# Optimization experiments

Hardware: AMD Instinct MI355X
Metric: run time of the kernel (lower is better)

## Reference

```python
import jax, jax.numpy as jnp
import numpy as np

B, T, L, D = 2, 16, 256, 1152
NH, HD = 16, 72
MLP_H = int(int(D * 4.0) * 2 / 3)  # 3072, per SwiGLUFFN


def _rms(x, w, eps=1e-6):
    return x * jax.lax.rsqrt(jnp.mean(jnp.square(x), axis=-1, keepdims=True) + eps) * w


def _attn(x, qkv_w, qkv_b, qn, kn, proj_w, proj_b, nh):
    Bn, N, C = x.shape
    hd = C // nh
    qkv = (x @ qkv_w + qkv_b).reshape(Bn, N, 3, nh, hd)
    qkv = jnp.transpose(qkv, (2, 0, 3, 1, 4))  # [3, Bn, nh, N, hd]
    q, k, v = qkv[0], qkv[1], qkv[2]
    q = _rms(q, qn)
    k = _rms(k, kn)
    scores = jnp.einsum('bhnd,bhmd->bhnm', q, k) / jnp.sqrt(jnp.float32(hd))
    a = jax.nn.softmax(scores, axis=-1)
    o = jnp.einsum('bhnm,bhmd->bhnd', a, v)
    o = jnp.transpose(o, (0, 2, 1, 3)).reshape(Bn, N, C)
    return o @ proj_w + proj_b


def setup_inputs() -> dict:
    key = jax.random.key(0)
    ks = jax.random.split(key, 12)
    w = lambda k, shape: jax.random.normal(k, shape, jnp.float32) * 0.02
    return {
        'x': jax.random.normal(ks[0], (B, T, L, D), jnp.float32),
        'c': jax.random.normal(ks[1], (B, D), jnp.float32),
        'norm1_w': jnp.ones((D,), jnp.float32),
        'norm2_w': jnp.ones((D,), jnp.float32),
        'norm3_w': jnp.ones((D,), jnp.float32),
        'qn_s': jnp.ones((HD,), jnp.float32),
        'kn_s': jnp.ones((HD,), jnp.float32),
        'qkv_s_w': w(ks[2], (D, 3 * D)),
        'qkv_s_b': jnp.zeros((3 * D,), jnp.float32),
        'proj_s_w': w(ks[3], (D, D)),
        'proj_s_b': jnp.zeros((D,), jnp.float32),
        'qn_t': jnp.ones((HD,), jnp.float32),
        'kn_t': jnp.ones((HD,), jnp.float32),
        'qkv_t_w': w(ks[4], (D, 3 * D)),
        'qkv_t_b': jnp.zeros((3 * D,), jnp.float32),
        'proj_t_w': w(ks[5], (D, D)),
        'proj_t_b': jnp.zeros((D,), jnp.float32),
        'w12_w': w(ks[6], (D, 2 * MLP_H)),
        'w12_b': jnp.zeros((2 * MLP_H,), jnp.float32),
        'w3_w': w(ks[7], (MLP_H, D)),
        'w3_b': jnp.zeros((D,), jnp.float32),
        'ada_w': w(ks[8], (D, 9 * D)),
        'ada_b': jnp.zeros((9 * D,), jnp.float32),
    }


def reference(x, c, norm1_w, norm2_w, norm3_w,
              qn_s, kn_s, qkv_s_w, qkv_s_b, proj_s_w, proj_s_b,
              qn_t, kn_t, qkv_t_w, qkv_t_b, proj_t_w, proj_t_b,
              w12_w, w12_b, w3_w, w3_b, ada_w, ada_b):
    Bb, Tt, Ll, Dd = x.shape
    # adaLN_modulation: SiLU then Linear, chunk into 9 [B, D] tensors
    ch = (jax.nn.silu(c) @ ada_w + ada_b).reshape(Bb, 9, Dd)
    sh_s, sc_s, g_s = ch[:, 0], ch[:, 1], ch[:, 2]
    sh_t, sc_t, g_t = ch[:, 3], ch[:, 4], ch[:, 5]
    sh_m, sc_m, g_m = ch[:, 6], ch[:, 7], ch[:, 8]

    # spatial attention over L, folded batch B*T
    x_s = x.reshape(Bb * Tt, Ll, Dd)
    shs = jnp.repeat(sh_s, Tt, axis=0)[:, None, :]   # [B*T,1,D]
    scs = jnp.repeat(sc_s, Tt, axis=0)[:, None, :]
    gs = jnp.repeat(g_s, Tt, axis=0)[:, None, :]
    xn = _rms(x_s, norm1_w) * (1 + scs) + shs
    x_s = x_s + gs * _attn(xn, qkv_s_w, qkv_s_b, qn_s, kn_s, proj_s_w, proj_s_b, NH)
    x = x_s.reshape(Bb, Tt, Ll, Dd)

    # temporal attention over T, folded batch B*L
    x_t = jnp.transpose(x, (0, 2, 1, 3)).reshape(Bb * Ll, Tt, Dd)
    sht = jnp.repeat(sh_t, Ll, axis=0)[:, None, :]
    sct = jnp.repeat(sc_t, Ll, axis=0)[:, None, :]
    gt = jnp.repeat(g_t, Ll, axis=0)[:, None, :]
    xn = _rms(x_t, norm2_w) * (1 + sct) + sht
    x_t = x_t + gt * _attn(xn, qkv_t_w, qkv_t_b, qn_t, kn_t, proj_t_w, proj_t_b, NH)
    x = jnp.transpose(x_t.reshape(Bb, Ll, Tt, Dd), (0, 2, 1, 3))

    # SwiGLU MLP with adaLN modulate + gate
    xn = _rms(x, norm3_w) * (1 + sc_m[:, None, None, :]) + sh_m[:, None, None, :]
    x12 = xn @ w12_w + w12_b
    x1, x2 = jnp.split(x12, 2, axis=-1)
    mlp_out = (jax.nn.silu(x1) * x2) @ w3_w + w3_b
    x = x + g_m[:, None, None, :] * mlp_out
    return x
```

## Files before the change

### kernel.cpp

```cpp
#include <hip/hip_runtime.h>
#include <stdint.h>

typedef __bf16 bf16x8 __attribute__((ext_vector_type(8)));
typedef float f32x4 __attribute__((ext_vector_type(4)));

__device__ __forceinline__ float b2f(uint32_t u) {
  union { uint32_t i; float f; } v; v.i = u << 16; return v.f;
}
__device__ __forceinline__ uint16_t f2b(float f) {
  union { float f; uint32_t i; } v; v.f = f;
  uint32_t r = (v.i + 0x7fffu + ((v.i >> 16) & 1u)) >> 16;
  return (uint16_t)r;
}
__device__ __forceinline__ void unpack8(uint4 u, float* f) {
  f[0] = b2f(u.x & 0xffffu); f[1] = b2f(u.x >> 16);
  f[2] = b2f(u.y & 0xffffu); f[3] = b2f(u.y >> 16);
  f[4] = b2f(u.z & 0xffffu); f[5] = b2f(u.z >> 16);
  f[6] = b2f(u.w & 0xffffu); f[7] = b2f(u.w >> 16);
}

__device__ __forceinline__ void gl2lds16(const void* g, void* l) {
  __builtin_amdgcn_global_load_lds(
      (const __attribute__((address_space(1))) void*)g,
      (__attribute__((address_space(3))) void*)l, 16, 0, 0);
}

__global__ __launch_bounds__(256) void gemm_k(
    const uint16_t* __restrict__ A, int lda,
    const uint16_t* __restrict__ Bt,
    const float* __restrict__ bias,
    uint16_t* __restrict__ outb,
    float* __restrict__ outf, const float* __restrict__ resid,
    const float* __restrict__ gate,
    int N, int K, int mode)
{
  __shared__ __align__(16) uint16_t As[2][128 * 32];
  __shared__ __align__(16) uint16_t Bs[2][128 * 32];
  const int tid = threadIdx.x;
  const int xcd = blockIdx.x & 7;
  const int slot = blockIdx.x >> 3;
  const int mt = xcd * 8 + (slot & 7);
  const int nt = slot >> 3;
  const int row0 = mt * 128, col0 = nt * 128;

  const int lane = tid & 63, wave = tid >> 6;
  const int l15 = lane & 15, quad = lane >> 4;
  const int wm = (wave & 1) * 64, wn = (wave >> 1) * 64;

  f32x4 acc[4][4];
  const f32x4 zero = {0.f, 0.f, 0.f, 0.f};
  for (int i = 0; i < 4; i++)
    for (int j = 0; j < 4; j++)
      acc[i][j] = zero;

  const int rseg = wave * 32 + (lane >> 2);
  const int kseg8 = (((lane & 3) ^ ((lane >> 2) & 3) ^ ((lane >> 4) & 3))) * 8;
  const uint16_t* gA = A + (size_t)(row0 + rseg) * lda + kseg8;
  const uint16_t* gB = Bt + (size_t)(col0 + rseg) * K + kseg8;
  const size_t rowA16 = (size_t)16 * lda;
  const size_t rowB16 = (size_t)16 * K;
  const int woff = wave * 2048;

  const int gsw = ((quad ^ (l15 & 3) ^ ((l15 >> 2) & 3))) * 8;

  gl2lds16(gA,          (char*)As[0] + woff);
  gl2lds16(gA + rowA16, (char*)As[0] + woff + 1024);
  gl2lds16(gB,          (char*)Bs[0] + woff);
  gl2lds16(gB + rowB16, (char*)Bs[0] + woff + 1024);

  for (int k0 = 0; k0 < K; k0 += 32) {
    const int cur = (k0 >> 5) & 1;
    __syncthreads();
    if (k0 + 32 < K) {
      const int nxt = cur ^ 1;
      gl2lds16(gA + k0 + 32,          (char*)As[nxt] + woff);
      gl2lds16(gA + rowA16 + k0 + 32, (char*)As[nxt] + woff + 1024);
      gl2lds16(gB + k0 + 32,          (char*)Bs[nxt] + woff);
      gl2lds16(gB + rowB16 + k0 + 32, (char*)Bs[nxt] + woff + 1024);
    }

    bf16x8 af[4], bfr[4];
#pragma unroll
    for (int i = 0; i < 4; i++) {
      af[i]  = *(const bf16x8*)&As[cur][(wm + i * 16 + l15) * 32 + gsw];
      bfr[i] = *(const bf16x8*)&Bs[cur][(wn + i * 16 + l15) * 32 + gsw];
    }
#pragma unroll
    for (int mi = 0; mi < 4; mi++)
#pragma unroll
      for (int ni = 0; ni < 4; ni++)
        acc[mi][ni] = __builtin_amdgcn_mfma_f32_16x16x32_bf16(af[mi], bfr[ni], acc[mi][ni], 0, 0, 0);
  }

#pragma unroll
  for (int mi = 0; mi < 4; mi++) {
#pragma unroll
    for (int ni = 0; ni < 4; ni++) {
      const int colg = col0 + wn + ni * 16 + l15;
      const float bv = bias ? bias[colg] : 0.f;
#pragma unroll
      for (int i = 0; i < 4; i++) {
        const int rowg = row0 + wm + mi * 16 + quad * 4 + i;
        const float v = acc[mi][ni][i] + bv;
        const size_t idx = (size_t)rowg * N + colg;
        if (mode == 0) {
          outb[idx] = f2b(v);
        } else {
          const int b = rowg >> 12;
          outf[idx] = resid[idx] + gate[b * 10368 + colg] * v;
        }
      }
    }
  }
}

__global__ __launch_bounds__(512, 2) void gemm256_k(
    const uint16_t* __restrict__ A, int lda,
    const uint16_t* __restrict__ Bt,
    const float* __restrict__ bias,
    uint16_t* __restrict__ outb,
    int N, int K)
{
  __shared__ __align__(16) uint16_t L[65536];
  const int tid = threadIdx.x;
  const int lane = tid & 63, wave = tid >> 6;
  const int l15 = lane & 15, quad = lane >> 4;
  const int wm = (wave >> 2) * 128, wn = (wave & 3) * 64;

  const int xcd = blockIdx.x & 7;
  const int slot = blockIdx.x >> 3;
  const int mt = xcd * 4 + (slot & 3);
  const int nt = slot >> 2;
  const int row0 = mt * 256, col0 = nt * 256;

  const int NTk = K >> 6;

  const uint16_t* Ag = A + (size_t)row0 * lda;
  const uint16_t* Bg = Bt + (size_t)col0 * K;

  const int sX = (lane & 7) ^ (lane >> 3);
  const int laneRowA = lane >> 3;
  const int laneK8A = sX * 8;
  const int laneRowB = 2 * (lane >> 3) + ((sX >> 2) & 1);
  const int laneK8B = (sX & 3) * 8;
  const int rA0 = ((wave * 16) & 63) + (((wave * 16) >> 6) << 7);
  const int rB0 = wave * 32;

#define STAGE_A(BUF, SUB, KT) do { \
    const uint16_t* g_ = Ag + (size_t)(rA0 + (SUB) * 64 + laneRowA) * lda + (size_t)(KT) * 64 + laneK8A; \
    uint16_t* l_ = (uint16_t*)&L[(BUF) * 32768 + (rA0 + (SUB) * 64) * 64]; \
    gl2lds16(g_, l_); \
    gl2lds16(g_ + (size_t)8 * lda, l_ + 512); \
  } while (0)

#define STAGE_B(BUF, HALF, KT) do { \
    const uint16_t* g_ = Bg + (size_t)(rB0 + laneRowB) * K + (size_t)(KT) * 64 + (HALF) * 32 + laneK8B; \
    uint16_t* l_ = (uint16_t*)&L[(BUF) * 32768 + 16384 + (HALF) * 8192 + rB0 * 32]; \
    gl2lds16(g_, l_); \
    gl2lds16(g_ + (size_t)16 * K, l_ + 512); \
  } while (0)

  f32x4 acc[8][4];
#pragma unroll
  for (int i = 0; i < 8; i++)
#pragma unroll
    for (int j = 0; j < 4; j++)
      acc[i][j] = (f32x4){0.f, 0.f, 0.f, 0.f};

  bf16x8 a_[4], b_[4];

#define PHASE(CUR, KK, QM, READB, STAGE_STMT, VM_STMT) do { \
    _Pragma("unroll") for (int mi = 0; mi < 4; mi++) \
      a_[mi] = *(const bf16x8*)&L[(CUR) * 32768 + (wm + (QM) * 64 + mi * 16 + l15) * 64 + \
                                  ((((KK) * 4 + quad) ^ (l15 & 7)) * 8)]; \
    if (READB) { \
      _Pragma("unroll") for (int ni = 0; ni < 4; ni++) \
        b_[ni] = *(const bf16x8*)&L[(CUR) * 32768 + 16384 + (KK) * 8192 + \
                                    ((wn >> 1) + ni * 8 + (l15 >> 1)) * 64 + \
                                    ((((((l15 & 1) << 2) | quad)) ^ (l15 >> 1)) * 8)]; \
    } \
    STAGE_STMT; \
    __builtin_amdgcn_sched_barrier(0); \
    __builtin_amdgcn_s_barrier(); \
    asm volatile("s_waitcnt lgkmcnt(0)" ::: "memory"); \
    __builtin_amdgcn_sched_barrier(0); \
    __builtin_amdgcn_s_setprio(1); \
    _Pragma("unroll") for (int mi = 0; mi < 4; mi++) \
      _Pragma("unroll") for (int ni = 0; ni < 4; ni++) \
        acc[(QM) * 4 + mi][ni] = __builtin_amdgcn_mfma_f32_16x16x32_bf16( \
            a_[mi], b_[ni], acc[(QM) * 4 + mi][ni], 0, 0, 0); \
    __builtin_amdgcn_s_setprio(0); \
    __builtin_amdgcn_sched_barrier(0); \
    VM_STMT; \
    __builtin_amdgcn_sched_barrier(0); \
    __builtin_amdgcn_s_barrier(); \
    __builtin_amdgcn_sched_barrier(0); \
  } while (0)

#define TILE(CUR, T) do { \
    PHASE(CUR, 0, 0, 1, { if ((T) + 1 < NTk) STAGE_B((CUR) ^ 1, 1, (T) + 1); }, {}); \
    PHASE(CUR, 0, 1, 0, { if ((T) + 1 < NTk) STAGE_A((CUR) ^ 1, 1, (T) + 1); }, {}); \
    PHASE(CUR, 1, 0, 1, { if ((T) + 2 < NTk) STAGE_B((CUR), 0, (T) + 2); }, {}); \
    PHASE(CUR, 1, 1, 0, { if ((T) + 2 < NTk) STAGE_A((CUR), 0, (T) + 2); }, \
      { if ((T) + 2 < NTk) { asm volatile("s_waitcnt vmcnt(4)" ::: "memory"); } \
        else               { asm volatile("s_waitcnt vmcnt(0)" ::: "memory"); } }); \
  } while (0)

  STAGE_A(0, 0, 0); STAGE_A(0, 1, 0); STAGE_B(0, 0, 0); STAGE_B(0, 1, 0);
  STAGE_A(1, 0, 1); STAGE_B(1, 0, 1);
  asm volatile("s_waitcnt vmcnt(4)" ::: "memory");
  __builtin_amdgcn_sched_barrier(0);
  __builtin_amdgcn_s_barrier();
  __builtin_amdgcn_sched_barrier(0);

  for (int t = 0; t < NTk; t += 2) {
    TILE(0, t);
    TILE(1, t + 1);
  }

#undef PHASE
#undef TILE
#undef STAGE_A
#undef STAGE_B

#pragma unroll
  for (int mi = 0; mi < 8; mi++) {
#pragma unroll
    for (int ni = 0; ni < 4; ni++) {
      const int colg = col0 + wn + ni * 16 + l15;
      const float bv = bias[colg];
#pragma unroll
      for (int i = 0; i < 4; i++) {
        const int rowg = row0 + wm + mi * 16 + quad * 4 + i;
        outb[(size_t)rowg * N + colg] = f2b(acc[mi][ni][i] + bv);
      }
    }
  }
}

__global__ __launch_bounds__(256) void rmsnorm_k(
    const float* __restrict__ x, const float* __restrict__ w,
    const float* __restrict__ chv, int shsel, int scsel,
    uint16_t* __restrict__ xn)
{
  const int row = blockIdx.x;
  const int b = row >> 12;
  const float* xr = x + (size_t)row * 1152;
  float ss = 0.f;
  for (int d = threadIdx.x; d < 1152; d += 256) { const float v = xr[d]; ss += v * v; }
  for (int off = 32; off > 0; off >>= 1) ss += __shfl_down(ss, off);
  __shared__ float red[4];
  if ((threadIdx.x & 63) == 0) red[threadIdx.x >> 6] = ss;
  __syncthreads();
  const float tot = red[0] + red[1] + red[2] + red[3];
  const float rs = rsqrtf(tot * (1.f / 1152.f) + 1e-6f);
  const float* sh = chv + b * 10368 + shsel * 1152;
  const float* sc = chv + b * 10368 + scsel * 1152;
  uint16_t* xo = xn + (size_t)row * 1152;
  for (int d = threadIdx.x; d < 1152; d += 256)
    xo[d] = f2b(xr[d] * rs * w[d] * (1.f + sc[d]) + sh[d]);
}

__global__ __launch_bounds__(256) void qknorm_k(
    uint16_t* __restrict__ qkv, const float* __restrict__ qn, const float* __restrict__ kn)
{
  const int tid = threadIdx.x;
  const int rl = tid >> 5, unit = tid & 31;
  const int h = unit & 15, isK = unit >> 4;
  const size_t row = (size_t)blockIdx.x * 8 + rl;
  uint16_t* p = qkv + row * 3456 + isK * 1152 + h * 72;
  const float* w = isK ? kn : qn;
  float v[72];
#pragma unroll
  for (int i = 0; i < 9; i++) unpack8(((const uint4*)p)[i], v + i * 8);
  float ss = 0.f;
#pragma unroll
  for (int d = 0; d < 72; d++) ss += v[d] * v[d];
  const float rs = rsqrtf(ss * (1.f / 72.f) + 1e-6f);
#pragma unroll
  for (int d = 0; d < 72; d++) p[d] = f2b(v[d] * rs * w[d]);
}

#define AK_STRIDE 104
#define VT_STRIDE 88
#define PS_STRIDE 72
__global__ __launch_bounds__(256) void attn_s_k(
    const uint16_t* __restrict__ qkv, uint16_t* __restrict__ out)
{
  __shared__ __align__(16) uint16_t Ks[64 * AK_STRIDE];
  __shared__ __align__(16) uint16_t Vt[80 * VT_STRIDE];
  __shared__ __align__(16) uint16_t Ps[4 * 64 * PS_STRIDE];
  const int bh = blockIdx.x;
  const int bt = bh >> 4, h = bh & 15;
  const int tid = threadIdx.x;
  const int lane = tid & 63, wave = tid >> 6;
  const int l15 = lane & 15, quad = lane >> 4;
  const size_t rowbase = (size_t)bt * 256;
  const float scale = 0.1178511301977579f;

  union { uint4 u; bf16x8 v; } zu; zu.u = make_uint4(0, 0, 0, 0);
  const bf16x8 zero8 = zu.v;

  bf16x8 qf[4][3];
#pragma unroll
  for (int mi = 0; mi < 4; mi++) {
    const uint16_t* qp = qkv + (rowbase + wave * 64 + mi * 16 + l15) * 3456 + h * 72;
    qf[mi][0] = *(const bf16x8*)(qp + quad * 8);
    qf[mi][1] = *(const bf16x8*)(qp + 32 + quad * 8);
    qf[mi][2] = (quad == 0) ? *(const bf16x8*)(qp + 64) : zero8;
  }

  f32x4 oacc[4][5];
#pragma unroll
  for (int mi = 0; mi < 4; mi++)
#pragma unroll
    for (int dt = 0; dt < 5; dt++)
      oacc[mi][dt] = (f32x4){0.f, 0.f, 0.f, 0.f};
  float mrun[4][4], lrun[4][4];
#pragma unroll
  for (int mi = 0; mi < 4; mi++)
#pragma unroll
    for (int i = 0; i < 4; i++) { mrun[mi][i] = -1e30f; lrun[mi][i] = 0.f; }

  uint16_t* psw = &Ps[wave * 64 * PS_STRIDE];

  for (int c = 0; c < 4; c++) {
    __syncthreads();
    for (int idx = tid; idx < 576; idx += 256) {
      const int rr = idx / 9, cc = idx - rr * 9;
      const uint16_t* kg = qkv + (rowbase + c * 64 + rr) * 3456 + 1152 + h * 72 + cc * 8;
      *(uint4*)&Ks[rr * AK_STRIDE + cc * 8] = *(const uint4*)kg;
      uint4 vv = *(const uint4*)(kg + 1152);
      const uint16_t* e = (const uint16_t*)&vv;
#pragma unroll
      for (int j = 0; j < 8; j++) Vt[(cc * 8 + j) * VT_STRIDE + rr] = e[j];
    }
    __syncthreads();

    f32x4 s[4][4];
#pragma unroll
    for (int mi = 0; mi < 4; mi++)
#pragma unroll
      for (int ni = 0; ni < 4; ni++)
        s[mi][ni] = (f32x4){0.f, 0.f, 0.f, 0.f};
#pragma unroll
    for (int ni = 0; ni < 4; ni++) {
      bf16x8 kf0 = *(const bf16x8*)&Ks[(ni * 16 + l15) * AK_STRIDE + quad * 8];
      bf16x8 kf1 = *(const bf16x8*)&Ks[(ni * 16 + l15) * AK_STRIDE + 32 + quad * 8];
      bf16x8 kf2 = (quad == 0) ? *(const bf16x8*)&Ks[(ni * 16 + l15) * AK_STRIDE + 64] : zero8;
#pragma unroll
      for (int mi = 0; mi < 4; mi++) {
        s[mi][ni] = __builtin_amdgcn_mfma_f32_16x16x32_bf16(qf[mi][0], kf0, s[mi][ni], 0, 0, 0);
        s[mi][ni] = __builtin_amdgcn_mfma_f32_16x16x32_bf16(qf[mi][1], kf1, s[mi][ni], 0, 0, 0);
        s[mi][ni] = __builtin_amdgcn_mfma_f32_16x16x32_bf16(qf[mi][2], kf2, s[mi][ni], 0, 0, 0);
      }
    }

#pragma unroll
    for (int mi = 0; mi < 4; mi++) {
#pragma unroll
      for (int i = 0; i < 4; i++) {
        float mx = fmaxf(fmaxf(s[mi][0][i], s[mi][1][i]), fmaxf(s[mi][2][i], s[mi][3][i])) * scale;
#pragma unroll
        for (int d = 1; d < 16; d <<= 1) mx = fmaxf(mx, __shfl_xor(mx, d));
        const float mnew = fmaxf(mrun[mi][i], mx);
        const float corr = __expf(mrun[mi][i] - mnew);
        mrun[mi][i] = mnew;
        float psum = 0.f;
#pragma unroll
        for (int ni = 0; ni < 4; ni++) {
          const float p = __expf(s[mi][ni][i] * scale - mnew);
          s[mi][ni][i] = p;
          psum += p;
        }
#pragma unroll
        for (int d = 1; d < 16; d <<= 1) psum += __shfl_xor(psum, d);
        lrun[mi][i] = lrun[mi][i] * corr + psum;
#pragma unroll
        for (int dt = 0; dt < 5; dt++) oacc[mi][dt][i] *= corr;
      }
    }

#pragma unroll
    for (int mi = 0; mi < 4; mi++)
#pragma unroll
      for (int ni = 0; ni < 4; ni++)
#pragma unroll
        for (int i = 0; i < 4; i++)
          psw[(mi * 16 + quad * 4 + i) * PS_STRIDE + ni * 16 + l15] = f2b(s[mi][ni][i]);

#pragma unroll
    for (int kk = 0; kk < 2; kk++) {
      bf16x8 pf[4];
#pragma unroll
      for (int mi = 0; mi < 4; mi++)
        pf[mi] = *(const bf16x8*)&psw[(mi * 16 + l15) * PS_STRIDE + kk * 32 + quad * 8];
#pragma unroll
      for (int dt = 0; dt < 5; dt++) {
        bf16x8 vf = *(const bf16x8*)&Vt[(dt * 16 + l15) * VT_STRIDE + kk * 32 + quad * 8];
#pragma unroll
        for (int mi = 0; mi < 4; mi++)
          oacc[mi][dt] = __builtin_amdgcn_mfma_f32_16x16x32_bf16(pf[mi], vf, oacc[mi][dt], 0, 0, 0);
      }
    }
  }

#pragma unroll
  for (int mi = 0; mi < 4; mi++) {
#pragma unroll
    for (int i = 0; i < 4; i++) {
      const float inv = 1.f / lrun[mi][i];
      const size_t orow = rowbase + wave * 64 + mi * 16 + quad * 4 + i;
#pragma unroll
      for (int dt = 0; dt < 5; dt++) {
        const int d = dt * 16 + l15;
        if (d < 72) out[orow * 1152 + h * 72 + d] = f2b(oacc[mi][dt][i] * inv);
      }
    }
  }
}

__global__ __launch_bounds__(128) void attn_t_k(
    const uint16_t* __restrict__ qkv, uint16_t* __restrict__ out)
{
  const int blk = blockIdx.x;
  const int bl = blk >> 1, hg = blk & 1;
  const int b = bl >> 8, l = bl & 255;
  const int tid = threadIdx.x;
  const int hh = tid >> 4, tq = tid & 15;
  const int h = hg * 8 + hh;
  __shared__ __align__(16) uint16_t kb[8 * 16 * 72];
  __shared__ __align__(16) uint16_t vb[8 * 16 * 72];

#pragma unroll
  for (int it = 0; it < 9; it++) {
    const int idx = tid + it * 128;
    const int rowL = idx / 9, cc = idx % 9;
    const int hhL = rowL >> 4, tL = rowL & 15;
    const size_t grow = (size_t)b * 4096 + (size_t)tL * 256 + l;
    const int colk = 1152 + (hg * 8 + hhL) * 72 + cc * 8;
    ((uint4*)&kb[rowL * 72])[cc] = *(const uint4*)(qkv + grow * 3456 + colk);
    ((uint4*)&vb[rowL * 72])[cc] = *(const uint4*)(qkv + grow * 3456 + colk + 1152);
  }
  __syncthreads();

  float q[72];
  const size_t qrow = (size_t)b * 4096 + (size_t)tq * 256 + l;
  {
    const uint16_t* qp = qkv + qrow * 3456 + h * 72;
#pragma unroll
    for (int i = 0; i < 9; i++) unpack8(((const uint4*)qp)[i], q + i * 8);
  }
  const float scale = 0.1178511301977579f;
  float s[16];
#pragma unroll
  for (int m = 0; m < 16; m++) {
    const uint4* kr = (const uint4*)&kb[(hh * 16 + m) * 72];
    float a = 0.f;
#pragma unroll
    for (int i = 0; i < 9; i++) {
      float kf[8]; unpack8(kr[i], kf);
#pragma unroll
      for (int j = 0; j < 8; j++) a += q[i * 8 + j] * kf[j];
    }
    s[m] = a * scale;
  }
  float mx = -1e30f;
#pragma unroll
  for (int m = 0; m < 16; m++) mx = fmaxf(mx, s[m]);
  float sum = 0.f;
#pragma unroll
  for (int m = 0; m < 16; m++) { s[m] = __expf(s[m] - mx); sum += s[m]; }
  const float inv = 1.f / sum;
  float o[72];
#pragma unroll
  for (int d = 0; d < 72; d++) o[d] = 0.f;
#pragma unroll
  for (int m = 0; m < 16; m++) {
    const float p = s[m];
    const uint4* vr = (const uint4*)&vb[(hh * 16 + m) * 72];
#pragma unroll
    for (int i = 0; i < 9; i++) {
      float vf[8]; unpack8(vr[i], vf);
#pragma unroll
      for (int j = 0; j < 8; j++) o[i * 8 + j] += p * vf[j];
    }
  }
  uint16_t* op = out + qrow * 1152 + h * 72;
#pragma unroll
  for (int d = 0; d < 72; d++) op[d] = f2b(o[d] * inv);
}

__global__ __launch_bounds__(256) void transcvt_k(
    const float* __restrict__ in, uint16_t* __restrict__ out, int K, int N)
{
  __shared__ float t[32][33];
  const int n0 = blockIdx.x * 32, k0 = blockIdx.y * 32;
  const int tx = threadIdx.x & 31, ty = threadIdx.x >> 5;
#pragma unroll
  for (int i = 0; i < 32; i += 8)
    t[ty + i][tx] = in[(size_t)(k0 + ty + i) * N + n0 + tx];
  __syncthreads();
#pragma unroll
  for (int i = 0; i < 32; i += 8)
    out[(size_t)(n0 + ty + i) * K + k0 + tx] = f2b(t[tx][ty + i]);
}

__global__ __launch_bounds__(256) void swiglu_k(uint16_t* __restrict__ x12)
{
  const size_t gid = (size_t)blockIdx.x * 256 + threadIdx.x;
  const size_t row = gid / 384, c8 = gid - row * 384;
  uint4* base = (uint4*)(x12 + row * 6144);
  float a[8], bb[8];
  unpack8(base[c8], a);
  unpack8(base[384 + c8], bb);
  uint32_t r[4];
#pragma unroll
  for (int j = 0; j < 4; j++) {
    const float s0 = a[2 * j]     / (1.f + __expf(-a[2 * j]))     * bb[2 * j];
    const float s1 = a[2 * j + 1] / (1.f + __expf(-a[2 * j + 1])) * bb[2 * j + 1];
    r[j] = (uint32_t)f2b(s0) | ((uint32_t)f2b(s1) << 16);
  }
  base[c8] = make_uint4(r[0], r[1], r[2], r[3]);
}

__global__ void siluc_k(const float* __restrict__ c, float* __restrict__ cs) {
  const int i = blockIdx.x * 256 + threadIdx.x;
  if (i < 2304) { const float v = c[i]; cs[i] = v / (1.f + __expf(-v)); }
}

#define ADA_KS 18
#define ADA_RK 64
__global__ __launch_bounds__(256) void ada_part_k(
    const float* __restrict__ cs, const float* __restrict__ W,
    float* __restrict__ part)
{
  const int col = blockIdx.x * 256 + threadIdx.x;
  const int ks = blockIdx.y;
  const int k0 = ks * ADA_RK;
  __shared__ float sc0[ADA_RK], sc1[ADA_RK];
  if (threadIdx.x < ADA_RK) sc0[threadIdx.x] = cs[k0 + threadIdx.x];
  else if (threadIdx.x < 2 * ADA_RK) sc1[threadIdx.x - ADA_RK] = cs[1152 + k0 + threadIdx.x - ADA_RK];
  __syncthreads();
  if (col >= 10368) return;
  const float* Wp = W + (size_t)k0 * 10368 + col;
  float s0 = 0.f, s1 = 0.f;
#pragma unroll 8
  for (int r = 0; r < ADA_RK; r++) {
    const float wv = Wp[(size_t)r * 10368];
    s0 += sc0[r] * wv;
    s1 += sc1[r] * wv;
  }
  part[(size_t)(ks * 2 + 0) * 10368 + col] = s0;
  part[(size_t)(ks * 2 + 1) * 10368 + col] = s1;
}

__global__ __launch_bounds__(256) void ada_reduce_k(
    const float* __restrict__ part, const float* __restrict__ bias,
    float* __restrict__ chv)
{
  const int col = blockIdx.x * 256 + threadIdx.x;
  if (col >= 10368) return;
  float s0 = bias[col], s1 = bias[col];
#pragma unroll
  for (int ks = 0; ks < ADA_KS; ks++) {
    s0 += part[(size_t)(ks * 2 + 0) * 10368 + col];
    s1 += part[(size_t)(ks * 2 + 1) * 10368 + col];
  }
  chv[col] = s0;
  chv[10368 + col] = s1;
}

extern "C" void kernel_launch(void* const* d_in, const int* in_sizes, int n_in,
                              void* d_out, int out_size, void* d_ws, size_t ws_size,
                              hipStream_t stream)
{
  const float* c_in    = (const float*)d_in[1];
  const float* norm1w  = (const float*)d_in[2];
  const float* norm2w  = (const float*)d_in[3];
  const float* norm3w  = (const float*)d_in[4];
  const float* qn_s    = (const float*)d_in[5];
  const float* kn_s    = (const float*)d_in[6];
  const float* qkv_s_w = (const float*)d_in[7];
  const float* qkv_s_b = (const float*)d_in[8];
  const float* proj_s_w= (const float*)d_in[9];
  const float* proj_s_b= (const float*)d_in[10];
  const float* qn_t    = (const float*)d_in[11];
  const float* kn_t    = (const float*)d_in[12];
  const float* qkv_t_w = (const float*)d_in[13];
  const float* qkv_t_b = (const float*)d_in[14];
  const float* proj_t_w= (const float*)d_in[15];
  const float* proj_t_b= (const float*)d_in[16];
  const float* w12_w   = (const float*)d_in[17];
  const float* w12_b   = (const float*)d_in[18];
  const float* w3_w    = (const float*)d_in[19];
  const float* w3_b    = (const float*)d_in[20];
  const float* ada_w   = (const float*)d_in[21];
  const float* ada_b   = (const float*)d_in[22];

  float* X = (float*)d_out;

  char* wsb = (char*)d_ws; size_t off = 0;
  auto alloc = [&](size_t bytes) -> void* {
    void* p = wsb + off; off += bytes; off = (off + 255) & ~(size_t)255; return p;
  };
  uint16_t* XN    = (uint16_t*)alloc((size_t)8192 * 1152 * 2);
  uint16_t* QKV   = (uint16_t*)alloc((size_t)8192 * 6144 * 2);
  uint16_t* X12   = QKV;
  uint16_t* WqkvS = (uint16_t*)alloc((size_t)3456 * 1152 * 2);
  uint16_t* WprojS= (uint16_t*)alloc((size_t)1152 * 1152 * 2);
  uint16_t* WqkvT = (uint16_t*)alloc((size_t)3456 * 1152 * 2);
  uint16_t* WprojT= (uint16_t*)alloc((size_t)1152 * 1152 * 2);
  uint16_t* W12T  = (uint16_t*)alloc((size_t)6144 * 1152 * 2);
  uint16_t* W3T   = (uint16_t*)alloc((size_t)1152 * 3072 * 2);
  float* CH = (float*)alloc((size_t)2 * 10368 * 4);
  float* CS = (float*)alloc((size_t)2 * 1152 * 4);
  float* APART = (float*)alloc((size_t)ADA_KS * 2 * 10368 * 4);

  hipMemcpyAsync(X, d_in[0], (size_t)8192 * 1152 * 4, hipMemcpyDeviceToDevice, stream);
  siluc_k<<<9, 256, 0, stream>>>(c_in, CS);
  ada_part_k<<<dim3(41, ADA_KS), 256, 0, stream>>>(CS, ada_w, APART);
  ada_reduce_k<<<41, 256, 0, stream>>>(APART, ada_b, CH);

  transcvt_k<<<dim3(3456 / 32, 1152 / 32), 256, 0, stream>>>(qkv_s_w, WqkvS, 1152, 3456);
  transcvt_k<<<dim3(1152 / 32, 1152 / 32), 256, 0, stream>>>(proj_s_w, WprojS, 1152, 1152);
  transcvt_k<<<dim3(3456 / 32, 1152 / 32), 256, 0, stream>>>(qkv_t_w, WqkvT, 1152, 3456);
  transcvt_k<<<dim3(1152 / 32, 1152 / 32), 256, 0, stream>>>(proj_t_w, WprojT, 1152, 1152);
  transcvt_k<<<dim3(6144 / 32, 1152 / 32), 256, 0, stream>>>(w12_w, W12T, 1152, 6144);
  transcvt_k<<<dim3(1152 / 32, 3072 / 32), 256, 0, stream>>>(w3_w, W3T, 3072, 1152);

  rmsnorm_k<<<8192, 256, 0, stream>>>(X, norm1w, CH, 0, 1, XN);
  gemm_k<<<27 * 64, 256, 0, stream>>>(XN, 1152, WqkvS, qkv_s_b, QKV, nullptr, nullptr, nullptr,
                                      3456, 1152, 0);
  qknorm_k<<<1024, 256, 0, stream>>>(QKV, qn_s, kn_s);
  attn_s_k<<<512, 256, 0, stream>>>(QKV, XN);
  gemm_k<<<9 * 64, 256, 0, stream>>>(XN, 1152, WprojS, proj_s_b, nullptr, X, X, CH + 2 * 1152,
                                     1152, 1152, 1);

  rmsnorm_k<<<8192, 256, 0, stream>>>(X, norm2w, CH, 3, 4, XN);
  gemm_k<<<27 * 64, 256, 0, stream>>>(XN, 1152, WqkvT, qkv_t_b, QKV, nullptr, nullptr, nullptr,
                                      3456, 1152, 0);
  qknorm_k<<<1024, 256, 0, stream>>>(QKV, qn_t, kn_t);
  attn_t_k<<<1024, 128, 0, stream>>>(QKV, XN);
  gemm_k<<<9 * 64, 256, 0, stream>>>(XN, 1152, WprojT, proj_t_b, nullptr, X, X, CH + 5 * 1152,
                                     1152, 1152, 1);

  rmsnorm_k<<<8192, 256, 0, stream>>>(X, norm3w, CH, 6, 7, XN);
  gemm256_k<<<32 * 24, 512, 0, stream>>>(XN, 1152, W12T, w12_b, X12, 6144, 1152);
  swiglu_k<<<12288, 256, 0, stream>>>(X12);
  gemm_k<<<9 * 64, 256, 0, stream>>>(X12, 6144, W3T, w3_b, nullptr, X, X, CH + 8 * 1152,
                                     1152, 3072, 1);
}
```

Measured before the change: 993.8 us.

## Fuse SwiGLU into W12 GEMM epilogue via interleaved weights; drop input copy

The W12 weight columns are interleaved during the transpose-convert, so each adjacent column pair holds x1 and x2. The GEMM epilogue can then compute silu(x1)*x2 with a lane shuffle and write only the 3072-wide hidden tensor. This removes the separate swiglu kernel and the full 6144-wide bf16 round trip. The initial device-to-device copy of x into the output is also dropped: the first rmsnorm reads the input directly and the spatial proj GEMM uses it as the residual, and rmsnorm is vectorized with float4 loads. Half the epilogue lanes now sit idle during the stores.

```diff
diff --git a/kernel.cpp b/kernel.cpp
--- a/kernel.cpp
+++ b/kernel.cpp
@@ -114,12 +114,12 @@
   }
 }
 
-__global__ __launch_bounds__(512, 2) void gemm256_k(
+__global__ __launch_bounds__(512, 2) void gemm256_sw_k(
     const uint16_t* __restrict__ A, int lda,
     const uint16_t* __restrict__ Bt,
     const float* __restrict__ bias,
-    uint16_t* __restrict__ outb,
-    int N, int K)
+    uint16_t* __restrict__ outh,
+    int K)
 {
   __shared__ __align__(16) uint16_t L[65536];
   const int tid = threadIdx.x;
@@ -228,11 +228,17 @@
 #pragma unroll
     for (int ni = 0; ni < 4; ni++) {
       const int colg = col0 + wn + ni * 16 + l15;
-      const float bv = bias[colg];
+      const float bv = bias[(colg & 1) * 3072 + (colg >> 1)];
+      const int hcol = ((col0 + wn + ni * 16) >> 1) + (l15 >> 1);
 #pragma unroll
       for (int i = 0; i < 4; i++) {
         const int rowg = row0 + wm + mi * 16 + quad * 4 + i;
-        outb[(size_t)rowg * N + colg] = f2b(acc[mi][ni][i] + bv);
+        const float v = acc[mi][ni][i] + bv;
+        const float o = __shfl_xor(v, 1);
+        if ((l15 & 1) == 0) {
+          const float hres = v / (1.f + __expf(-v)) * o;
+          outh[(size_t)rowg * 3072 + hcol] = f2b(hres);
+        }
       }
     }
   }
@@ -245,20 +251,38 @@
 {
   const int row = blockIdx.x;
   const int b = row >> 12;
-  const float* xr = x + (size_t)row * 1152;
-  float ss = 0.f;
-  for (int d = threadIdx.x; d < 1152; d += 256) { const float v = xr[d]; ss += v * v; }
+  const int tid = threadIdx.x;
+  const float4* x4 = (const float4*)(x + (size_t)row * 1152);
+  float4 a = x4[tid];
+  float ss = a.x * a.x + a.y * a.y + a.z * a.z + a.w * a.w;
+  float4 a2 = {0.f, 0.f, 0.f, 0.f};
+  if (tid < 32) {
+    a2 = x4[256 + tid];
+    ss += a2.x * a2.x + a2.y * a2.y + a2.z * a2.z + a2.w * a2.w;
+  }
   for (int off = 32; off > 0; off >>= 1) ss += __shfl_down(ss, off);
   __shared__ float red[4];
-  if ((threadIdx.x & 63) == 0) red[threadIdx.x >> 6] = ss;
+  if ((tid & 63) == 0) red[tid >> 6] = ss;
   __syncthreads();
   const float tot = red[0] + red[1] + red[2] + red[3];
   const float rs = rsqrtf(tot * (1.f / 1152.f) + 1e-6f);
-  const float* sh = chv + b * 10368 + shsel * 1152;
-  const float* sc = chv + b * 10368 + scsel * 1152;
-  uint16_t* xo = xn + (size_t)row * 1152;
-  for (int d = threadIdx.x; d < 1152; d += 256)
-    xo[d] = f2b(xr[d] * rs * w[d] * (1.f + sc[d]) + sh[d]);
+  const float4* w4 = (const float4*)w;
+  const float4* sh4 = (const float4*)(chv + b * 10368 + shsel * 1152);
+  const float4* sc4 = (const float4*)(chv + b * 10368 + scsel * 1152);
+  uint2* xo = (uint2*)(xn + (size_t)row * 1152);
+  auto proc = [&](float4 av, int idx) {
+    const float4 wv = w4[idx], shv = sh4[idx], scv = sc4[idx];
+    const float r0 = av.x * rs * wv.x * (1.f + scv.x) + shv.x;
+    const float r1 = av.y * rs * wv.y * (1.f + scv.y) + shv.y;
+    const float r2 = av.z * rs * wv.z * (1.f + scv.z) + shv.z;
+    const float r3 = av.w * rs * wv.w * (1.f + scv.w) + shv.w;
+    uint2 o;
+    o.x = (uint32_t)f2b(r0) | ((uint32_t)f2b(r1) << 16);
+    o.y = (uint32_t)f2b(r2) | ((uint32_t)f2b(r3) << 16);
+    xo[idx] = o;
+  };
+  proc(a, tid);
+  if (tid < 32) proc(a2, 256 + tid);
 }
 
 __global__ __launch_bounds__(256) void qknorm_k(
@@ -506,22 +530,20 @@
     out[(size_t)(n0 + ty + i) * K + k0 + tx] = f2b(t[tx][ty + i]);
 }
 
-__global__ __launch_bounds__(256) void swiglu_k(uint16_t* __restrict__ x12)
-{
-  const size_t gid = (size_t)blockIdx.x * 256 + threadIdx.x;
-  const size_t row = gid / 384, c8 = gid - row * 384;
-  uint4* base = (uint4*)(x12 + row * 6144);
-  float a[8], bb[8];
-  unpack8(base[c8], a);
-  unpack8(base[384 + c8], bb);
-  uint32_t r[4];
-#pragma unroll
-  for (int j = 0; j < 4; j++) {
-    const float s0 = a[2 * j]     / (1.f + __expf(-a[2 * j]))     * bb[2 * j];
-    const float s1 = a[2 * j + 1] / (1.f + __expf(-a[2 * j + 1])) * bb[2 * j + 1];
-    r[j] = (uint32_t)f2b(s0) | ((uint32_t)f2b(s1) << 16);
-  }
-  base[c8] = make_uint4(r[0], r[1], r[2], r[3]);
+__global__ __launch_bounds__(256) void transcvt_w12i_k(
+    const float* __restrict__ in, uint16_t* __restrict__ out)
+{
+  __shared__ float t[32][33];
+  const int n0 = blockIdx.x * 32, k0 = blockIdx.y * 32;
+  const int tx = threadIdx.x & 31, ty = threadIdx.x >> 5;
+  const int scol = ((tx & 1) * 3072) + (n0 >> 1) + (tx >> 1);
+#pragma unroll
+  for (int i = 0; i < 32; i += 8)
+    t[ty + i][tx] = in[(size_t)(k0 + ty + i) * 6144 + scol];
+  __syncthreads();
+#pragma unroll
+  for (int i = 0; i < 32; i += 8)
+    out[(size_t)(n0 + ty + i) * 1152 + k0 + tx] = f2b(t[tx][ty + i]);
 }
 
 __global__ void siluc_k(const float* __restrict__ c, float* __restrict__ cs) {
@@ -575,6 +597,7 @@
                               void* d_out, int out_size, void* d_ws, size_t ws_size,
                               hipStream_t stream)
 {
+  const float* Xin     = (const float*)d_in[0];
   const float* c_in    = (const float*)d_in[1];
   const float* norm1w  = (const float*)d_in[2];
   const float* norm2w  = (const float*)d_in[3];
@@ -605,8 +628,8 @@
     void* p = wsb + off; off += bytes; off = (off + 255) & ~(size_t)255; return p;
   };
   uint16_t* XN    = (uint16_t*)alloc((size_t)8192 * 1152 * 2);
-  uint16_t* QKV   = (uint16_t*)alloc((size_t)8192 * 6144 * 2);
-  uint16_t* X12   = QKV;
+  uint16_t* QKV   = (uint16_t*)alloc((size_t)8192 * 3456 * 2);
+  uint16_t* H     = QKV;
   uint16_t* WqkvS = (uint16_t*)alloc((size_t)3456 * 1152 * 2);
   uint16_t* WprojS= (uint16_t*)alloc((size_t)1152 * 1152 * 2);
   uint16_t* WqkvT = (uint16_t*)alloc((size_t)3456 * 1152 * 2);
@@ -617,7 +640,6 @@
   float* CS = (float*)alloc((size_t)2 * 1152 * 4);
   float* APART = (float*)alloc((size_t)ADA_KS * 2 * 10368 * 4);
 
-  hipMemcpyAsync(X, d_in[0], (size_t)8192 * 1152 * 4, hipMemcpyDeviceToDevice, stream);
   siluc_k<<<9, 256, 0, stream>>>(c_in, CS);
   ada_part_k<<<dim3(41, ADA_KS), 256, 0, stream>>>(CS, ada_w, APART);
   ada_reduce_k<<<41, 256, 0, stream>>>(APART, ada_b, CH);
@@ -626,15 +648,15 @@
   transcvt_k<<<dim3(1152 / 32, 1152 / 32), 256, 0, stream>>>(proj_s_w, WprojS, 1152, 1152);
   transcvt_k<<<dim3(3456 / 32, 1152 / 32), 256, 0, stream>>>(qkv_t_w, WqkvT, 1152, 3456);
   transcvt_k<<<dim3(1152 / 32, 1152 / 32), 256, 0, stream>>>(proj_t_w, WprojT, 1152, 1152);
-  transcvt_k<<<dim3(6144 / 32, 1152 / 32), 256, 0, stream>>>(w12_w, W12T, 1152, 6144);
+  transcvt_w12i_k<<<dim3(6144 / 32, 1152 / 32), 256, 0, stream>>>(w12_w, W12T);
   transcvt_k<<<dim3(1152 / 32, 3072 / 32), 256, 0, stream>>>(w3_w, W3T, 3072, 1152);
 
-  rmsnorm_k<<<8192, 256, 0, stream>>>(X, norm1w, CH, 0, 1, XN);
+  rmsnorm_k<<<8192, 256, 0, stream>>>(Xin, norm1w, CH, 0, 1, XN);
   gemm_k<<<27 * 64, 256, 0, stream>>>(XN, 1152, WqkvS, qkv_s_b, QKV, nullptr, nullptr, nullptr,
                                       3456, 1152, 0);
   qknorm_k<<<1024, 256, 0, stream>>>(QKV, qn_s, kn_s);
   attn_s_k<<<512, 256, 0, stream>>>(QKV, XN);
-  gemm_k<<<9 * 64, 256, 0, stream>>>(XN, 1152, WprojS, proj_s_b, nullptr, X, X, CH + 2 * 1152,
+  gemm_k<<<9 * 64, 256, 0, stream>>>(XN, 1152, WprojS, proj_s_b, nullptr, X, Xin, CH + 2 * 1152,
                                      1152, 1152, 1);
 
   rmsnorm_k<<<8192, 256, 0, stream>>>(X, norm2w, CH, 3, 4, XN);
@@ -646,8 +668,7 @@
                                      1152, 1152, 1);
 
   rmsnorm_k<<<8192, 256, 0, stream>>>(X, norm3w, CH, 6, 7, XN);
-  gemm256_k<<<32 * 24, 512, 0, stream>>>(XN, 1152, W12T, w12_b, X12, 6144, 1152);
-  swiglu_k<<<12288, 256, 0, stream>>>(X12);
-  gemm_k<<<9 * 64, 256, 0, stream>>>(X12, 6144, W3T, w3_b, nullptr, X, X, CH + 8 * 1152,
+  gemm256_sw_k<<<32 * 24, 512, 0, stream>>>(XN, 1152, W12T, w12_b, H, 1152);
+  gemm_k<<<9 * 64, 256, 0, stream>>>(H, 3072, W3T, w3_b, nullptr, X, X, CH + 8 * 1152,
                                      1152, 3072, 1);
 }
```

After: 976.1 us. No clear change (-1.8%).
